# Kernel optimization log

Measured on AMD Instinct MI355X. Metric: run time of the kernel, lower is better.

The kernel has to match this reference:

```python
import jax, jax.numpy as jnp
import numpy as np

NUM_STATES = 512
NUM_OBS = 1024
BATCH = 64
T = 512


def setup_inputs() -> dict:
    key = jax.random.key(0)
    k_obs, k_pi, k_A, k_B = jax.random.split(key, 4)
    observations = jax.random.randint(k_obs, (BATCH, T), 0, NUM_OBS, dtype=jnp.int32)
    log_pi = jax.random.normal(k_pi, (NUM_STATES,), dtype=jnp.float32)
    log_A = jax.random.normal(k_A, (NUM_STATES, NUM_STATES), dtype=jnp.float32)
    log_B = jax.random.normal(k_B, (NUM_STATES, NUM_OBS), dtype=jnp.float32)
    return {"observations": observations, "log_pi": log_pi, "log_A": log_A, "log_B": log_B}


def _hmm_loglik(observations, log_pi, log_A, log_B):
    # Normalize parameters in log-space (as in the torch module).
    lpi = jax.nn.log_softmax(log_pi, axis=0)            # (S,)
    lA = jax.nn.log_softmax(log_A, axis=1)              # (S, S)
    lB = jax.nn.log_softmax(log_B, axis=1)              # (S, O)

    # Emission log-probs per timestep: (B, T, S)
    emit = lB.T[observations]                            # gather columns of lB

    alpha0 = lpi[None, :] + emit[:, 0, :]                # (B, S)

    def step(alpha, emit_t):
        # alpha: (B, S) over previous state i; transition lA[i, j]
        alpha_next = jax.scipy.special.logsumexp(alpha[:, :, None] + lA[None, :, :], axis=1) + emit_t
        return alpha_next, None

    # scan over time axis; emit[:, 1:, :] -> (T-1, B, S)
    alpha_T, _ = jax.lax.scan(step, alpha0, jnp.swapaxes(emit[:, 1:, :], 0, 1))
    log_probs = jax.scipy.special.logsumexp(alpha_T, axis=1)  # (B,)
    return log_probs.sum()


def reference(observations, log_pi, log_A, log_B):
    return _hmm_loglik(observations, log_pi, log_A, log_B)
```

## Files before the change

kernel.cpp:

```cpp
#include <hip/hip_runtime.h>

#define S     512
#define NOBS  1024
#define TT    512
#define CH    16
#define NWAVE 4
#define NJT   8
#define NGRP  4

typedef __attribute__((ext_vector_type(4))) float f32x4;
typedef __attribute__((ext_vector_type(4))) int   i32x4;
typedef __attribute__((ext_vector_type(8))) int   i32x8;
typedef __attribute__((ext_vector_type(2))) unsigned int u32x2;
typedef long i64;

__device__ __forceinline__ unsigned short f2bf(float x) {
  unsigned u = __builtin_bit_cast(unsigned, x);
  return (unsigned short)((u + 0x7fffu + ((u >> 16) & 1u)) >> 16);
}
__device__ __forceinline__ float bflo(unsigned u) {
  return __builtin_bit_cast(float, u << 16);
}
__device__ __forceinline__ float bfhi_raw(unsigned u) {
  return __builtin_bit_cast(float, u);
}
__device__ __forceinline__ float bfhi(unsigned u) {
  return __builtin_bit_cast(float, u & 0xffff0000u);
}

__device__ __forceinline__ unsigned char f2fp8_sw(float x) {
  x = fminf(fmaxf(x, 0.f), 448.f);
  unsigned u = __builtin_bit_cast(unsigned, x);
  int ex = (int)((u >> 23) & 0xff);
  if (ex >= 121) {
    unsigned m = (u & 0x7fffff) | 0x800000;
    unsigned keep = m >> 20, rest = m & 0xfffff;
    keep += (rest > 0x80000u) || (rest == 0x80000u && (keep & 1));
    int e8 = ex - 127 + 7;
    if (keep == 16) { keep = 8; e8++; }
    if (e8 >= 16) return 0x7e;
    return (unsigned char)((e8 << 3) | (keep & 7));
  } else {
    int m = (int)(x * 512.0f + 0.5f);
    if (m > 8) m = 8;
    return (unsigned char)m;
  }
}

__device__ __forceinline__ unsigned pack4_fp8(float p0, float p1, float p2, float p3) {
#if __has_builtin(__builtin_amdgcn_cvt_pk_fp8_f32)
  int v = __builtin_amdgcn_cvt_pk_fp8_f32(p0, p1, 0, false);
  v = __builtin_amdgcn_cvt_pk_fp8_f32(p2, p3, v, true);
  return (unsigned)v;
#else
  return (unsigned)f2fp8_sw(p0) | ((unsigned)f2fp8_sw(p1) << 8) |
         ((unsigned)f2fp8_sw(p2) << 16) | ((unsigned)f2fp8_sw(p3) << 24);
#endif
}

__device__ __forceinline__ float wave_max(float v) {
  for (int d = 32; d; d >>= 1) v = fmaxf(v, __shfl_xor(v, d));
  return v;
}
__device__ __forceinline__ float wave_sum(float v) {
  for (int d = 32; d; d >>= 1) v += __shfl_xor(v, d);
  return v;
}

__global__ void prep_pi(const float* __restrict__ log_pi, float* __restrict__ lpi) {
  const int l = threadIdx.x;
  float v[8];
  float mx = -INFINITY;
  for (int k = 0; k < 8; ++k) { v[k] = log_pi[l + 64 * k]; mx = fmaxf(mx, v[k]); }
  mx = wave_max(mx);
  float sm = 0.f;
  for (int k = 0; k < 8; ++k) sm += __expf(v[k] - mx);
  sm = wave_sum(sm);
  const float lse = mx + __logf(sm);
  for (int k = 0; k < 8; ++k) lpi[l + 64 * k] = v[k] - lse;
}

__global__ void prep_B(const float* __restrict__ log_B, unsigned short* __restrict__ Bexp16) {
  const int j = blockIdx.x, l = threadIdx.x;
  const float* row = log_B + (size_t)j * NOBS;
  float v[16];
  float mx = -INFINITY;
  for (int k = 0; k < 16; ++k) { v[k] = row[l + 64 * k]; mx = fmaxf(mx, v[k]); }
  mx = wave_max(mx);
  float sm = 0.f;
  for (int k = 0; k < 16; ++k) sm += __expf(v[k] - mx);
  sm = wave_sum(sm);
  const float lse = mx + __logf(sm);
  for (int k = 0; k < 16; ++k) Bexp16[(size_t)(l + 64 * k) * S + j] = f2bf(__expf(v[k] - lse));
}

__global__ void prep_A(const float* __restrict__ log_A, unsigned char* __restrict__ Afrag8) {
  const int i = blockIdx.x, l = threadIdx.x;
  const float* row = log_A + (size_t)i * S;
  float v[8];
  float mx = -INFINITY;
  for (int k = 0; k < 8; ++k) { v[k] = row[l + 64 * k]; mx = fmaxf(mx, v[k]); }
  mx = wave_max(mx);
  float sm = 0.f;
  for (int k = 0; k < 8; ++k) sm += __expf(v[k] - mx);
  sm = wave_sum(sm);
  const float lse = mx + __logf(sm);
  const int c = i >> 7, g4s = (i >> 5) & 3, e = i & 31;
  for (int k = 0; k < 8; ++k) {
    const int j = l + 64 * k;
    const int jt = j >> 4, jc = j & 15;
    Afrag8[((size_t)(jt * 4 + c) * 64 + g4s * 16 + jc) * 32 + e] = f2fp8_sw(__expf(v[k] - lse));
  }
}

__device__ __forceinline__ int pswz(int m, int g) { return m * 512 + (((g ^ m) & 31) << 4); }

__device__ __forceinline__ float max4(const float* p) {
  const f32x4 v = *reinterpret_cast<const f32x4*>(p);
  return fmaxf(fmaxf(v[0], v[1]), fmaxf(v[2], v[3]));
}
__device__ __forceinline__ float sum4(const float* p) {
  const f32x4 v = *reinterpret_cast<const f32x4*>(p);
  return (v[0] + v[1]) + (v[2] + v[3]);
}

__device__ __forceinline__ f32x4 mfma_chunk(const i32x8 a, const i32x8 b, f32x4 acc) {
#if __has_builtin(__builtin_amdgcn_mfma_scale_f32_16x16x128_f8f6f4)
  return __builtin_amdgcn_mfma_scale_f32_16x16x128_f8f6f4(
             a, b, acc, 0, 0, 0, 0x7f7f7f7f, 0, 0x7f7f7f7f);
#else
  const i64* pa = reinterpret_cast<const i64*>(&a);
  const i64* pb = reinterpret_cast<const i64*>(&b);
  #pragma unroll
  for (int q = 0; q < 4; ++q)
    acc = __builtin_amdgcn_mfma_f32_16x16x32_fp8_fp8(pa[q], pb[q], acc, 0, 0, 0);
  return acc;
#endif
}

__global__ __launch_bounds__(256, 1)
void hmm_main(const int* __restrict__ obs, const float* __restrict__ lpi,
              const unsigned short* __restrict__ Bexp16,
              const unsigned char* __restrict__ Afrag8, float* __restrict__ parts)
{
  __shared__ __align__(16) unsigned char Pb[2][CH * S];
  __shared__ int obs_s[CH][TT + 1];
  __shared__ __align__(16) float pred[2][CH][12];

  const int tid = threadIdx.x;
  const int w = tid >> 6, l = tid & 63, g4 = l >> 4, mm = l & 15;
  const int grp = blockIdx.x;

  i32x8 a_frags[NJT][4];
  #pragma unroll
  for (int ji = 0; ji < NJT; ++ji) {
    const int jt = w + NWAVE * ji;
    #pragma unroll
    for (int cc = 0; cc < 4; ++cc) {
      const int c = (cc + w) & 3;
      a_frags[ji][cc] = *reinterpret_cast<const i32x8*>(
          Afrag8 + ((size_t)(jt * 4 + c) * 64 + l) * 32);
    }
  }

  int rd[4][2], wr[NJT];
  #pragma unroll
  for (int cc = 0; cc < 4; ++cc) {
    const int g0 = ((cc + w) & 3) * 8 + g4 * 2;
    rd[cc][0] = pswz(mm, g0);
    rd[cc][1] = pswz(mm, g0 + 1);
  }
  #pragma unroll
  for (int ji = 0; ji < NJT; ++ji) wr[ji] = pswz(mm, w + NWAVE * ji) + g4 * 4;

  for (int m = 0; m < CH; ++m) {
    obs_s[m][tid]       = obs[(size_t)(grp * CH + m) * TT + tid];
    obs_s[m][tid + 256] = obs[(size_t)(grp * CH + m) * TT + tid + 256];
  }
  __syncthreads();

  float lsc_f;
  int   lsc_i = 0;
  float Lp, e1p;

  {
    const int o0 = obs_s[mm][0];
    f32x4 vals[NJT];
    #pragma unroll
    for (int ji = 0; ji < NJT; ++ji) {
      const int j0 = (w + NWAVE * ji) * 16 + g4 * 4;
      const f32x4 lp = *reinterpret_cast<const f32x4*>(lpi + j0);
      const u32x2 e = *reinterpret_cast<const u32x2*>(Bexp16 + (size_t)o0 * S + j0);
      vals[ji][0] = lp[0] + __logf(bflo(e[0]));
      vals[ji][1] = lp[1] + __logf(bfhi(e[0]));
      vals[ji][2] = lp[2] + __logf(bflo(e[1]));
      vals[ji][3] = lp[3] + __logf(bfhi(e[1]));
    }
    float v = -INFINITY;
    #pragma unroll
    for (int ji = 0; ji < NJT; ++ji)
      v = fmaxf(v, fmaxf(fmaxf(vals[ji][0], vals[ji][1]), fmaxf(vals[ji][2], vals[ji][3])));
    v = fmaxf(v, __shfl_xor(v, 16));
    v = fmaxf(v, __shfl_xor(v, 32));
    if (g4 == 0) pred[0][mm][w] = v;
    __syncthreads();
    const float M0 = max4(&pred[0][mm][0]);
    #pragma unroll
    for (int ji = 0; ji < NJT; ++ji)
      *reinterpret_cast<unsigned*>(&Pb[0][wr[ji]]) =
          pack4_fp8(__expf(vals[ji][0] - M0), __expf(vals[ji][1] - M0),
                    __expf(vals[ji][2] - M0), __expf(vals[ji][3] - M0));
    lsc_f = M0;
    __syncthreads();
  }

  {
    const int o1 = obs_s[mm][1];
    u32x2 eb[NJT];
    const unsigned short* bp = Bexp16 + ((size_t)o1 << 9) + g4 * 4 + w * 16;
    #pragma unroll
    for (int ji = 0; ji < NJT; ++ji)
      eb[ji] = *reinterpret_cast<const u32x2*>(bp + ji * 64);

    f32x4 acc[NJT];
    #pragma unroll
    for (int ji = 0; ji < NJT; ++ji) acc[ji] = f32x4{0.f, 0.f, 0.f, 0.f};
    #pragma unroll
    for (int cc = 0; cc < 4; ++cc) {
      i32x8 af;
      i32x4* h = reinterpret_cast<i32x4*>(&af);
      h[0] = *reinterpret_cast<const i32x4*>(&Pb[0][rd[cc][0]]);
      h[1] = *reinterpret_cast<const i32x4*>(&Pb[0][rd[cc][1]]);
      #pragma unroll
      for (int ji = 0; ji < NJT; ++ji)
        acc[ji] = mfma_chunk(a_frags[ji][cc], af, acc[ji]);
    }
    f32x4 vals[NJT];
    #pragma unroll
    for (int ji = 0; ji < NJT; ++ji) {
      vals[ji][0] = acc[ji][0] * bflo(eb[ji][0]);
      vals[ji][1] = acc[ji][1] * bfhi(eb[ji][0]);
      vals[ji][2] = acc[ji][2] * bflo(eb[ji][1]);
      vals[ji][3] = acc[ji][3] * bfhi(eb[ji][1]);
    }
    float v = -INFINITY;
    #pragma unroll
    for (int ji = 0; ji < NJT; ++ji)
      v = fmaxf(v, fmaxf(fmaxf(vals[ji][0], vals[ji][1]), fmaxf(vals[ji][2], vals[ji][3])));
    v = fmaxf(v, __shfl_xor(v, 16));
    v = fmaxf(v, __shfl_xor(v, 32));
    if (g4 == 0) pred[1][mm][w] = v;
    __syncthreads();
    const float v1 = max4(&pred[1][mm][0]);
    const float inv = __builtin_amdgcn_rcpf(v1);
    lsc_f += __logf(v1);
    Lp = __log2f(v1); e1p = 0.f;
    #pragma unroll
    for (int ji = 0; ji < NJT; ++ji)
      *reinterpret_cast<unsigned*>(&Pb[1][wr[ji]]) =
          pack4_fp8(vals[ji][0] * inv, vals[ji][1] * inv,
                    vals[ji][2] * inv, vals[ji][3] * inv);
    __syncthreads();
  }

  for (int t = 2; t < TT - 1; ++t) {
    const int cur = t & 1;
    const unsigned char* __restrict__ pprv = Pb[cur ^ 1];
    unsigned char* __restrict__ pcur = Pb[cur];

    const int ob = obs_s[mm][t];
    u32x2 eb[NJT];
    const unsigned short* bp = Bexp16 + ((size_t)ob << 9) + g4 * 4 + w * 16;
    #pragma unroll
    for (int ji = 0; ji < NJT; ++ji)
      eb[ji] = *reinterpret_cast<const u32x2*>(bp + ji * 64);

    const float pm = max4(&pred[cur ^ 1][mm][0]);

    f32x4 acc[NJT];
    #pragma unroll
    for (int ji = 0; ji < NJT; ++ji) acc[ji] = f32x4{0.f, 0.f, 0.f, 0.f};
    #pragma unroll
    for (int cc = 0; cc < 4; ++cc) {
      i32x8 af;
      i32x4* h = reinterpret_cast<i32x4*>(&af);
      h[0] = *reinterpret_cast<const i32x4*>(pprv + rd[cc][0]);
      h[1] = *reinterpret_cast<const i32x4*>(pprv + rd[cc][1]);
      #pragma unroll
      for (int ji = 0; ji < NJT; ++ji)
        acc[ji] = mfma_chunk(a_frags[ji][cc], af, acc[ji]);
    }

    const float e_new = (t == 2) ? 0.f : __log2f(pm);
    const float dsr = fminf(fmaxf(e_new - e1p, -3.0f), 3.0f);
    int s = (int)__builtin_rintf(Lp + e_new + dsr);
    s = min(max(s, -60), 60);
    Lp = (float)s; e1p = e_new; lsc_i += s;
    const float pw2 = __builtin_bit_cast(float, (unsigned)(127 - s) << 23);

    float vmax = 0.f;
    #pragma unroll
    for (int ji = 0; ji < NJT; ++ji) {
      const float q0 = acc[ji][0] * (bflo(eb[ji][0]) * pw2);
      const float q1 = acc[ji][1] * (bfhi_raw(eb[ji][0]) * pw2);
      const float q2 = acc[ji][2] * (bflo(eb[ji][1]) * pw2);
      const float q3 = acc[ji][3] * (bfhi_raw(eb[ji][1]) * pw2);
      *reinterpret_cast<unsigned*>(pcur + wr[ji]) = pack4_fp8(q0, q1, q2, q3);
      vmax = fmaxf(fmaxf(vmax, fmaxf(fmaxf(q0, q1), q2)), q3);
    }
    vmax = fmaxf(vmax, __shfl_xor(vmax, 16));
    vmax = fmaxf(vmax, __shfl_xor(vmax, 32));
    if (g4 == 0) pred[cur][mm][w] = vmax;
    __syncthreads();
  }

  {
    const int t = TT - 1, cur = t & 1;
    const unsigned char* __restrict__ pprv = Pb[cur ^ 1];
    const int ob = obs_s[mm][t];
    u32x2 eb[NJT];
    const unsigned short* bp = Bexp16 + ((size_t)ob << 9) + g4 * 4 + w * 16;
    #pragma unroll
    for (int ji = 0; ji < NJT; ++ji)
      eb[ji] = *reinterpret_cast<const u32x2*>(bp + ji * 64);
    const float pm = max4(&pred[cur ^ 1][mm][0]);

    f32x4 acc[NJT];
    #pragma unroll
    for (int ji = 0; ji < NJT; ++ji) acc[ji] = f32x4{0.f, 0.f, 0.f, 0.f};
    #pragma unroll
    for (int cc = 0; cc < 4; ++cc) {
      i32x8 af;
      i32x4* h = reinterpret_cast<i32x4*>(&af);
      h[0] = *reinterpret_cast<const i32x4*>(pprv + rd[cc][0]);
      h[1] = *reinterpret_cast<const i32x4*>(pprv + rd[cc][1]);
      #pragma unroll
      for (int ji = 0; ji < NJT; ++ji)
        acc[ji] = mfma_chunk(a_frags[ji][cc], af, acc[ji]);
    }

    const float e_new = __log2f(pm);
    const float dsr = fminf(fmaxf(e_new - e1p, -3.0f), 3.0f);
    int s = (int)__builtin_rintf(Lp + e_new + dsr);
    s = min(max(s, -60), 60);
    lsc_i += s;
    const float pw2 = __builtin_bit_cast(float, (unsigned)(127 - s) << 23);

    float ssum = 0.f;
    #pragma unroll
    for (int ji = 0; ji < NJT; ++ji)
      ssum += acc[ji][0] * bflo(eb[ji][0]) + acc[ji][1] * bfhi(eb[ji][0]) +
              acc[ji][2] * bflo(eb[ji][1]) + acc[ji][3] * bfhi(eb[ji][1]);
    ssum *= pw2;
    ssum += __shfl_xor(ssum, 16);
    ssum += __shfl_xor(ssum, 32);
    if (g4 == 0) pred[cur][mm][w] = ssum;
    __syncthreads();
    if (w == 0 && g4 == 0) {
      const float s4 = sum4(&pred[cur][mm][0]);
      float cl = lsc_f + (float)lsc_i * 0.69314718056f + __logf(s4);
      for (int d = 1; d < 16; d <<= 1) cl += __shfl_xor(cl, d);
      if (l == 0) parts[grp] = cl;
    }
  }
}

__global__ void final_sum(const float* __restrict__ parts, float* __restrict__ out) {
  out[0] = parts[0] + parts[1] + parts[2] + parts[3];
}

extern "C" void kernel_launch(void* const* d_in, const int* in_sizes, int n_in,
                              void* d_out, int out_size, void* d_ws, size_t ws_size,
                              hipStream_t stream) {
  const int*   obs  = (const int*)d_in[0];
  const float* lgpi = (const float*)d_in[1];
  const float* lgA  = (const float*)d_in[2];
  const float* lgB  = (const float*)d_in[3];
  float* out = (float*)d_out;

  char* ws = (char*)d_ws;
  unsigned short* Bexp16 = (unsigned short*)ws;
  unsigned char*  Afrag8 = (unsigned char*)(ws + (size_t)NOBS * S * 2);
  float*          lpi    = (float*)(ws + (size_t)NOBS * S * 2 + (size_t)S * S);
  float*          parts  = lpi + S;

  prep_pi<<<1, 64, 0, stream>>>(lgpi, lpi);
  prep_B<<<S, 64, 0, stream>>>(lgB, Bexp16);
  prep_A<<<S, 64, 0, stream>>>(lgA, Afrag8);
  hmm_main<<<NGRP, 256, 0, stream>>>(obs, lpi, Bexp16, Afrag8, parts);
  final_sum<<<1, 1, 0, stream>>>(parts, out);
}
```

Measured before the change: 836.4 us.

## Split per-step state tiles across eight waves instead of four

Doubles the block size to 512 threads, so each wave owns 4 state tiles instead of 8. This halves the per-wave MFMA chain and register-held A fragments in each serial time step. Cross-wave max and sum reductions now combine 8 partial values, and the observation staging loop is adjusted. The cost is a wider barrier across 8 waves every step and a tighter register budget from the new launch bounds.

```diff
diff --git a/kernel.cpp b/kernel.cpp
--- a/kernel.cpp
+++ b/kernel.cpp
@@ -4,8 +4,8 @@
 #define NOBS  1024
 #define TT    512
 #define CH    16
-#define NWAVE 4
-#define NJT   8
+#define NWAVE 8
+#define NJT   4
 #define NGRP  4
 
 typedef __attribute__((ext_vector_type(4))) float f32x4;
@@ -115,13 +115,16 @@
 
 __device__ __forceinline__ int pswz(int m, int g) { return m * 512 + (((g ^ m) & 31) << 4); }
 
-__device__ __forceinline__ float max4(const float* p) {
-  const f32x4 v = *reinterpret_cast<const f32x4*>(p);
-  return fmaxf(fmaxf(v[0], v[1]), fmaxf(v[2], v[3]));
-}
-__device__ __forceinline__ float sum4(const float* p) {
-  const f32x4 v = *reinterpret_cast<const f32x4*>(p);
-  return (v[0] + v[1]) + (v[2] + v[3]);
+__device__ __forceinline__ float max8(const float* p) {
+  const f32x4 p0 = *reinterpret_cast<const f32x4*>(p);
+  const f32x4 p1 = *reinterpret_cast<const f32x4*>(p + 4);
+  return fmaxf(fmaxf(fmaxf(p0[0], p0[1]), fmaxf(p0[2], p0[3])),
+               fmaxf(fmaxf(p1[0], p1[1]), fmaxf(p1[2], p1[3])));
+}
+__device__ __forceinline__ float sum8(const float* p) {
+  const f32x4 p0 = *reinterpret_cast<const f32x4*>(p);
+  const f32x4 p1 = *reinterpret_cast<const f32x4*>(p + 4);
+  return ((p0[0] + p0[1]) + (p0[2] + p0[3])) + ((p1[0] + p1[1]) + (p1[2] + p1[3]));
 }
 
 __device__ __forceinline__ f32x4 mfma_chunk(const i32x8 a, const i32x8 b, f32x4 acc) {
@@ -138,7 +141,7 @@
 #endif
 }
 
-__global__ __launch_bounds__(256, 1)
+__global__ __launch_bounds__(512, 2)
 void hmm_main(const int* __restrict__ obs, const float* __restrict__ lpi,
               const unsigned short* __restrict__ Bexp16,
               const unsigned char* __restrict__ Afrag8, float* __restrict__ parts)
@@ -173,10 +176,8 @@
   #pragma unroll
   for (int ji = 0; ji < NJT; ++ji) wr[ji] = pswz(mm, w + NWAVE * ji) + g4 * 4;
 
-  for (int m = 0; m < CH; ++m) {
-    obs_s[m][tid]       = obs[(size_t)(grp * CH + m) * TT + tid];
-    obs_s[m][tid + 256] = obs[(size_t)(grp * CH + m) * TT + tid + 256];
-  }
+  for (int m = 0; m < CH; ++m)
+    obs_s[m][tid] = obs[(size_t)(grp * CH + m) * TT + tid];
   __syncthreads();
 
   float lsc_f;
@@ -204,7 +205,7 @@
     v = fmaxf(v, __shfl_xor(v, 32));
     if (g4 == 0) pred[0][mm][w] = v;
     __syncthreads();
-    const float M0 = max4(&pred[0][mm][0]);
+    const float M0 = max8(&pred[0][mm][0]);
     #pragma unroll
     for (int ji = 0; ji < NJT; ++ji)
       *reinterpret_cast<unsigned*>(&Pb[0][wr[ji]]) =
@@ -220,7 +221,7 @@
     const unsigned short* bp = Bexp16 + ((size_t)o1 << 9) + g4 * 4 + w * 16;
     #pragma unroll
     for (int ji = 0; ji < NJT; ++ji)
-      eb[ji] = *reinterpret_cast<const u32x2*>(bp + ji * 64);
+      eb[ji] = *reinterpret_cast<const u32x2*>(bp + ji * 128);
 
     f32x4 acc[NJT];
     #pragma unroll
@@ -251,7 +252,7 @@
     v = fmaxf(v, __shfl_xor(v, 32));
     if (g4 == 0) pred[1][mm][w] = v;
     __syncthreads();
-    const float v1 = max4(&pred[1][mm][0]);
+    const float v1 = max8(&pred[1][mm][0]);
     const float inv = __builtin_amdgcn_rcpf(v1);
     lsc_f += __logf(v1);
     Lp = __log2f(v1); e1p = 0.f;
@@ -273,9 +274,9 @@
     const unsigned short* bp = Bexp16 + ((size_t)ob << 9) + g4 * 4 + w * 16;
     #pragma unroll
     for (int ji = 0; ji < NJT; ++ji)
-      eb[ji] = *reinterpret_cast<const u32x2*>(bp + ji * 64);
-
-    const float pm = max4(&pred[cur ^ 1][mm][0]);
+      eb[ji] = *reinterpret_cast<const u32x2*>(bp + ji * 128);
+
+    const float pm = max8(&pred[cur ^ 1][mm][0]);
 
     f32x4 acc[NJT];
     #pragma unroll
@@ -322,8 +323,8 @@
     const unsigned short* bp = Bexp16 + ((size_t)ob << 9) + g4 * 4 + w * 16;
     #pragma unroll
     for (int ji = 0; ji < NJT; ++ji)
-      eb[ji] = *reinterpret_cast<const u32x2*>(bp + ji * 64);
-    const float pm = max4(&pred[cur ^ 1][mm][0]);
+      eb[ji] = *reinterpret_cast<const u32x2*>(bp + ji * 128);
+    const float pm = max8(&pred[cur ^ 1][mm][0]);
 
     f32x4 acc[NJT];
     #pragma unroll
@@ -357,8 +358,8 @@
     if (g4 == 0) pred[cur][mm][w] = ssum;
     __syncthreads();
     if (w == 0 && g4 == 0) {
-      const float s4 = sum4(&pred[cur][mm][0]);
-      float cl = lsc_f + (float)lsc_i * 0.69314718056f + __logf(s4);
+      const float s8 = sum8(&pred[cur][mm][0]);
+      float cl = lsc_f + (float)lsc_i * 0.69314718056f + __logf(s8);
       for (int d = 1; d < 16; d <<= 1) cl += __shfl_xor(cl, d);
       if (l == 0) parts[grp] = cl;
     }
@@ -387,6 +388,6 @@
   prep_pi<<<1, 64, 0, stream>>>(lgpi, lpi);
   prep_B<<<S, 64, 0, stream>>>(lgB, Bexp16);
   prep_A<<<S, 64, 0, stream>>>(lgA, Afrag8);
-  hmm_main<<<NGRP, 256, 0, stream>>>(obs, lpi, Bexp16, Afrag8, parts);
+  hmm_main<<<NGRP, 512, 0, stream>>>(obs, lpi, Bexp16, Afrag8, parts);
   final_sum<<<1, 1, 0, stream>>>(parts, out);
 }
```

New measurement: 701.2 us. -16.2%, faster.
